# Kernel optimization log

Measured on AMD Instinct MI355X. Metric: run time of the kernel, lower is better.

Reference implementation:

```python
import jax, jax.numpy as jnp
import numpy as np

IN_FEATURES = 128
OUT_FEATURES = 64

def setup_inputs() -> dict:
    key = jax.random.key(0)
    k1, k2, k3 = jax.random.split(key, 3)
    x = jax.random.normal(k1, (8, 4096, IN_FEATURES), dtype=jnp.float32)
    # nn.Linear weights: W [out, in], a [1, 2*out]
    W = jax.random.normal(k2, (OUT_FEATURES, IN_FEATURES), dtype=jnp.float32) / np.sqrt(IN_FEATURES)
    a = jax.random.normal(k3, (1, 2 * OUT_FEATURES), dtype=jnp.float32) / np.sqrt(2 * OUT_FEATURES)
    return {"x": x, "W": W, "a": a}

def reference(x, W, a):
    # h = x @ W.T : [B, N, D]
    h = jnp.einsum('bnf,df->bnd', x, W)
    d = h.shape[-1]
    a1 = a[0, :d]  # [D]
    a2 = a[0, d:]  # [D]
    score1 = h @ a1  # [B, N]
    score2 = h @ a2  # [B, N]
    # outer-sum broadcast: e[b,i,j] = leakyrelu(score1[b,i] + score2[b,j])
    e = jax.nn.leaky_relu(score1[:, :, None] + score2[:, None, :], negative_slope=0.2)
    attention = jax.nn.softmax(e, axis=-1)  # [B, N, N]
    h_prime = jnp.einsum('bij,bjd->bid', attention, h)
    return jax.nn.elu(h_prime)
```

## Files before the change

### kernel.cpp

```cpp
#include <hip/hip_runtime.h>
#include <hip/hip_bf16.h>

#define BB 8
#define NN 4096
#define FF 128
#define DD 64
#define NB (BB*NN)
#define CHK 128
#define NCH (NN/CHK)
#define CSZ 16
#define NC16 (NN/CSZ)
#define CH 72

#define OFF_H     0
#define OFF_S1    (OFF_H    + (size_t)NB*DD*4)
#define OFF_S2    (OFF_S1   + (size_t)NB*4)
#define OFF_S2S   (OFF_S2   + (size_t)NB*4)
#define OFF_PERM  (OFF_S2S  + (size_t)NB*4)
#define OFF_WPOS  (OFF_PERM + (size_t)NB*4)
#define OFF_WNEG  (OFF_WPOS + (size_t)NB*4)
#define OFF_CT16  (OFF_WNEG + (size_t)NB*4)
#define OFF_CTS   (OFF_CT16 + (size_t)BB*NC16*2*CH*8)
#define OFF_PRANK (OFF_CTS  + (size_t)BB*(NC16+1)*2*CH*8)

__device__ __forceinline__ unsigned int fkey(float f) {
  unsigned int u = __float_as_uint(f);
  return (u & 0x80000000u) ? ~u : (u | 0x80000000u);
}

__global__ __launch_bounds__(256) void gat_kA(const float* __restrict__ x,
                                              const float* __restrict__ W,
                                              const float* __restrict__ a,
                                              float* __restrict__ h,
                                              float* __restrict__ s1,
                                              float* __restrict__ s2) {
  __shared__ float xs[64][FF];
  const int tid  = threadIdx.x;
  const int lane = tid & 63;
  const int wave = tid >> 6;
  const long long rowbase = (long long)blockIdx.x * 64;

  const float4* x4  = (const float4*)(x + rowbase * FF);
  float4*       xs4 = (float4*)&xs[0][0];
#pragma unroll
  for (int i = 0; i < 8; ++i) xs4[tid + i * 256] = x4[tid + i * 256];

  float4 wreg[32];
  const float4* W4 = (const float4*)(W + lane * FF);
#pragma unroll
  for (int j = 0; j < 32; ++j) wreg[j] = W4[j];
  const float a1d = a[lane];
  const float a2d = a[DD + lane];
  __syncthreads();

  for (int r = wave * 16; r < wave * 16 + 16; ++r) {
    const float4* xr = (const float4*)&xs[r][0];
    float4 acc = {0.f, 0.f, 0.f, 0.f};
#pragma unroll
    for (int j = 0; j < 32; ++j) {
      float4 xv = xr[j];
      acc.x += xv.x * wreg[j].x;
      acc.y += xv.y * wreg[j].y;
      acc.z += xv.z * wreg[j].z;
      acc.w += xv.w * wreg[j].w;
    }
    float hd = (acc.x + acc.y) + (acc.z + acc.w);
    const long long row = rowbase + r;
    h[row * DD + lane] = hd;

    float p1 = hd * a1d, p2 = hd * a2d;
#pragma unroll
    for (int o = 32; o; o >>= 1) { p1 += __shfl_xor(p1, o); p2 += __shfl_xor(p2, o); }
    if (lane == 0) { s1[row] = p1; s2[row] = p2; }
  }
}

__global__ __launch_bounds__(256) void gat_kB1(const float* __restrict__ s2,
                                               unsigned short* __restrict__ prank) {
  __shared__ unsigned long long ks[CHK];
  const int c = blockIdx.x, b = blockIdx.y, tid = threadIdx.x;
  const float* s2b = s2 + (size_t)b * NN;

  if (tid < CHK) {
    const int ig = c * CHK + tid;
    ks[tid] = ((unsigned long long)fkey(s2b[ig]) << 12) | (unsigned)ig;
  }

  unsigned long long kj[16];
  int rank[16];
#pragma unroll
  for (int t = 0; t < 16; ++t) {
    const int j = tid + 256 * t;
    kj[t] = ((unsigned long long)fkey(s2b[j]) << 12) | (unsigned)j;
    rank[t] = 0;
  }
  __syncthreads();

#pragma unroll 4
  for (int i = 0; i < CHK; ++i) {
    const unsigned long long ki = ks[i];
#pragma unroll
    for (int t = 0; t < 16; ++t) rank[t] += (ki < kj[t]) ? 1 : 0;
  }

  unsigned short* pr = prank + ((size_t)c * BB + b) * NN;
#pragma unroll
  for (int t = 0; t < 16; ++t) pr[tid + 256 * t] = (unsigned short)rank[t];
}

__global__ __launch_bounds__(256) void gat_kB2(const float* __restrict__ s2,
                                               const unsigned short* __restrict__ prank,
                                               float* __restrict__ s2s,
                                               int* __restrict__ perm,
                                               float* __restrict__ wpos,
                                               float* __restrict__ wneg) {
  __shared__ float red[4];
  const int b = blockIdx.y, tid = threadIdx.x;
  const int j = blockIdx.x * 256 + tid;
  const float* s2b = s2 + (size_t)b * NN;

  float mx = -3.4e38f;
  for (int i = tid; i < NN; i += 256) mx = fmaxf(mx, s2b[i]);
#pragma unroll
  for (int o = 32; o; o >>= 1) mx = fmaxf(mx, __shfl_xor(mx, o));
  if ((tid & 63) == 0) red[tid >> 6] = mx;
  __syncthreads();
  mx = fmaxf(fmaxf(red[0], red[1]), fmaxf(red[2], red[3]));

  int rank = 0;
#pragma unroll 8
  for (int c = 0; c < NCH; ++c) rank += prank[((size_t)c * BB + b) * NN + j];

  const float key = s2b[j];
  const size_t o = (size_t)b * NN + rank;
  s2s[o]  = key;
  perm[o] = j;
  wpos[o] = expf(key - mx);
  wneg[o] = expf(0.2f * (key - mx));
}

__global__ __launch_bounds__(64) void gat_kC(const float* __restrict__ h,
                                             const int* __restrict__ perm,
                                             const float* __restrict__ wpos,
                                             const float* __restrict__ wneg,
                                             double* __restrict__ CT16) {
  const int c = blockIdx.x, b = blockIdx.y, d = threadIdx.x;
  const int base = b * NN + c * CSZ;
  double ap = 0, an = 0, zp = 0, zn = 0;
#pragma unroll
  for (int s = 0; s < CSZ; ++s) {
    const int j  = base + s;
    const int pj = perm[j];
    const float hv = h[((size_t)b * NN + pj) * DD + d];
    const float wp = wpos[j], wn = wneg[j];
    ap += (double)wp * hv; an += (double)wn * hv;
    zp += wp;              zn += wn;
  }
  double* o = CT16 + ((size_t)(b * NC16 + c) * 2) * CH;
  o[0 * CH + d] = an;
  o[1 * CH + d] = ap;
  if (d == 0) { o[0 * CH + 64] = zn; o[1 * CH + 64] = zp; }
}

__global__ __launch_bounds__(256) void gat_kD(const double* __restrict__ CT16,
                                              double* __restrict__ CTS) {
  const int b = blockIdx.x, t = threadIdx.x;
  const int fam = t >> 7, ch = t & 127;
  if (ch > 64) return;
  double off = 0;
#pragma unroll 4
  for (int c = 0; c < NC16; ++c) {
    CTS[(((size_t)b * (NC16 + 1) + c) * 2 + fam) * CH + ch] = off;
    off += CT16[(((size_t)b * NC16 + c) * 2 + fam) * CH + ch];
  }
  CTS[(((size_t)b * (NC16 + 1) + NC16) * 2 + fam) * CH + ch] = off;
}

__global__ __launch_bounds__(256) void gat_kF(const float* __restrict__ s1,
                                              const float* __restrict__ s2s,
                                              const int* __restrict__ perm,
                                              const float* __restrict__ wpos,
                                              const float* __restrict__ wneg,
                                              const float* __restrict__ h,
                                              const double* __restrict__ CTS,
                                              float* __restrict__ out) {
  __shared__ float key[NN];
  __shared__ float seglast[64];
  const int b = blockIdx.y;
  const int tid = threadIdx.x, lane = tid & 63, wv = tid >> 6;

  const float4* src = (const float4*)(s2s + (size_t)b * NN);
  float4* dst = (float4*)key;
#pragma unroll
  for (int i = 0; i < 4; ++i) dst[tid + 256 * i] = src[tid + 256 * i];
  __syncthreads();
  if (tid < 64) seglast[tid] = key[tid * 64 + 63];
  __syncthreads();

  const float c1 = key[NN - 1];
  const double* base0 = CTS + ((size_t)b * (NC16 + 1)) * 2 * CH;
  const double* tt = base0 + (size_t)NC16 * 2 * CH + CH;
  const double tot = tt[lane];
  const double Zt  = tt[64];
  const int bNN = b * NN;
  const float segl = seglast[lane];

  for (int r = 0; r < 4; ++r) {
    const int rowl = blockIdx.x * 16 + wv * 4 + r;
    const long long row = (long long)bNN + rowl;
    const float s1i = s1[row];
    const float t = -s1i;

    unsigned long long m1 = __ballot(segl <= t);
    int seg = __popcll(m1); if (seg > 63) seg = 63;
    const float v2 = key[seg * 64 + lane];
    unsigned long long m2 = __ballot(v2 <= t);
    const int k = seg * 64 + __popcll(m2);
    const int c16 = k >> 4;

    const double* r0 = base0 + (size_t)c16 * 2 * CH;
    const double* r1 = r0 + CH;
    double pre  = r0[lane];
    double p1v  = r1[lane];
    double Zpre = r0[64];
    double Z1   = r1[64];

    for (int j = (c16 << 4); j < k; ++j) {
      const int pj = perm[bNN + j];
      const float hv = h[((size_t)(bNN + pj)) * DD + lane];
      const float wp = wpos[bNN + j], wn = wneg[bNN + j];
      pre += (double)wn * hv; p1v += (double)wp * hv;
      Zpre += wn;             Z1 += wp;
    }

    const float suf_d = (float)(tot - p1v);
    const float Zsuf  = (float)(Zt - Z1);
    const float z = s1i + c1;
    const float m = z >= 0.f ? z : 0.2f * z;
    const float A  = expf(z - m);
    const float Bn = expf(0.2f * z - m);
    const float num = A * suf_d + Bn * (float)pre;
    const float Z   = A * Zsuf  + Bn * (float)Zpre;
    const float hp  = num / Z;
    out[row * DD + lane] = hp > 0.f ? hp : expm1f(hp);
  }
}

extern "C" void kernel_launch(void* const* d_in, const int* in_sizes, int n_in,
                              void* d_out, int out_size, void* d_ws, size_t ws_size,
                              hipStream_t stream) {
  const float* x = (const float*)d_in[0];
  const float* W = (const float*)d_in[1];
  const float* a = (const float*)d_in[2];
  float* out = (float*)d_out;

  char* ws = (char*)d_ws;
  float*  h    = (float*)(ws + OFF_H);
  float*  s1   = (float*)(ws + OFF_S1);
  float*  s2   = (float*)(ws + OFF_S2);
  float*  s2s  = (float*)(ws + OFF_S2S);
  int*    perm = (int*)  (ws + OFF_PERM);
  float*  wpos = (float*)(ws + OFF_WPOS);
  float*  wneg = (float*)(ws + OFF_WNEG);
  double* CT16 = (double*)(ws + OFF_CT16);
  double* CTS  = (double*)(ws + OFF_CTS);
  unsigned short* prank = (unsigned short*)(ws + OFF_PRANK);

  gat_kA<<<NB / 64, 256, 0, stream>>>(x, W, a, h, s1, s2);
  gat_kB1<<<dim3(NCH, BB), 256, 0, stream>>>(s2, prank);
  gat_kB2<<<dim3(NN / 256, BB), 256, 0, stream>>>(s2, prank, s2s, perm, wpos, wneg);
  gat_kC<<<dim3(NC16, BB), 64, 0, stream>>>(h, perm, wpos, wneg, CT16);
  gat_kD<<<BB, 256, 0, stream>>>(CT16, CTS);
  gat_kF<<<dim3(NN / 16, BB), 256, 0, stream>>>(s1, s2s, perm, wpos, wneg, h, CTS, out);
}
```

Before: 101.8 us.

## Pack perm and weight into int2, derive wpos from wneg, unroll tail loop

```diff
diff --git a/kernel.cpp b/kernel.cpp
--- a/kernel.cpp
+++ b/kernel.cpp
@@ -16,10 +16,8 @@
 #define OFF_S1    (OFF_H    + (size_t)NB*DD*4)
 #define OFF_S2    (OFF_S1   + (size_t)NB*4)
 #define OFF_S2S   (OFF_S2   + (size_t)NB*4)
-#define OFF_PERM  (OFF_S2S  + (size_t)NB*4)
-#define OFF_WPOS  (OFF_PERM + (size_t)NB*4)
-#define OFF_WNEG  (OFF_WPOS + (size_t)NB*4)
-#define OFF_CT16  (OFF_WNEG + (size_t)NB*4)
+#define OFF_PK    (OFF_S2S  + (size_t)NB*4)
+#define OFF_CT16  (OFF_PK   + (size_t)NB*8)
 #define OFF_CTS   (OFF_CT16 + (size_t)BB*NC16*2*CH*8)
 #define OFF_PRANK (OFF_CTS  + (size_t)BB*(NC16+1)*2*CH*8)
 
@@ -111,9 +109,7 @@
 __global__ __launch_bounds__(256) void gat_kB2(const float* __restrict__ s2,
                                                const unsigned short* __restrict__ prank,
                                                float* __restrict__ s2s,
-                                               int* __restrict__ perm,
-                                               float* __restrict__ wpos,
-                                               float* __restrict__ wneg) {
+                                               int2* __restrict__ pk) {
   __shared__ float red[4];
   const int b = blockIdx.y, tid = threadIdx.x;
   const int j = blockIdx.x * 256 + tid;
@@ -132,29 +128,27 @@
   for (int c = 0; c < NCH; ++c) rank += prank[((size_t)c * BB + b) * NN + j];
 
   const float key = s2b[j];
+  const float wn = expf(0.2f * (key - mx));
   const size_t o = (size_t)b * NN + rank;
-  s2s[o]  = key;
-  perm[o] = j;
-  wpos[o] = expf(key - mx);
-  wneg[o] = expf(0.2f * (key - mx));
+  s2s[o] = key;
+  pk[o]  = make_int2(j, __float_as_int(wn));
 }
 
 __global__ __launch_bounds__(64) void gat_kC(const float* __restrict__ h,
-                                             const int* __restrict__ perm,
-                                             const float* __restrict__ wpos,
-                                             const float* __restrict__ wneg,
+                                             const int2* __restrict__ pk,
                                              double* __restrict__ CT16) {
   const int c = blockIdx.x, b = blockIdx.y, d = threadIdx.x;
   const int base = b * NN + c * CSZ;
   double ap = 0, an = 0, zp = 0, zn = 0;
 #pragma unroll
   for (int s = 0; s < CSZ; ++s) {
-    const int j  = base + s;
-    const int pj = perm[j];
-    const float hv = h[((size_t)b * NN + pj) * DD + d];
-    const float wp = wpos[j], wn = wneg[j];
-    ap += (double)wp * hv; an += (double)wn * hv;
-    zp += wp;              zn += wn;
+    const int2 p = pk[base + s];
+    const float hv = h[((size_t)(b * NN + p.x)) * DD + d];
+    const float wn = __int_as_float(p.y);
+    const float w2 = wn * wn;
+    const float wp = w2 * w2 * wn;
+    an += (double)wn * hv; ap += (double)wp * hv;
+    zn += wn;              zp += wp;
   }
   double* o = CT16 + ((size_t)(b * NC16 + c) * 2) * CH;
   o[0 * CH + d] = an;
@@ -162,13 +156,12 @@
   if (d == 0) { o[0 * CH + 64] = zn; o[1 * CH + 64] = zp; }
 }
 
-__global__ __launch_bounds__(256) void gat_kD(const double* __restrict__ CT16,
+__global__ __launch_bounds__(128) void gat_kD(const double* __restrict__ CT16,
                                               double* __restrict__ CTS) {
-  const int b = blockIdx.x, t = threadIdx.x;
-  const int fam = t >> 7, ch = t & 127;
+  const int b = blockIdx.x, fam = blockIdx.y, ch = threadIdx.x;
   if (ch > 64) return;
   double off = 0;
-#pragma unroll 4
+#pragma unroll 16
   for (int c = 0; c < NC16; ++c) {
     CTS[(((size_t)b * (NC16 + 1) + c) * 2 + fam) * CH + ch] = off;
     off += CT16[(((size_t)b * NC16 + c) * 2 + fam) * CH + ch];
@@ -178,9 +171,7 @@
 
 __global__ __launch_bounds__(256) void gat_kF(const float* __restrict__ s1,
                                               const float* __restrict__ s2s,
-                                              const int* __restrict__ perm,
-                                              const float* __restrict__ wpos,
-                                              const float* __restrict__ wneg,
+                                              const int2* __restrict__ pk,
                                               const float* __restrict__ h,
                                               const double* __restrict__ CTS,
                                               float* __restrict__ out) {
@@ -197,26 +188,29 @@
   if (tid < 64) seglast[tid] = key[tid * 64 + 63];
   __syncthreads();
 
+  const int bNN = b * NN;
   const float c1 = key[NN - 1];
   const double* base0 = CTS + ((size_t)b * (NC16 + 1)) * 2 * CH;
   const double* tt = base0 + (size_t)NC16 * 2 * CH + CH;
   const double tot = tt[lane];
   const double Zt  = tt[64];
-  const int bNN = b * NN;
   const float segl = seglast[lane];
 
+  float s1v[4];
+#pragma unroll
+  for (int r = 0; r < 4; ++r) s1v[r] = s1[bNN + blockIdx.x * 16 + wv * 4 + r];
+
+#pragma unroll
   for (int r = 0; r < 4; ++r) {
     const int rowl = blockIdx.x * 16 + wv * 4 + r;
-    const long long row = (long long)bNN + rowl;
-    const float s1i = s1[row];
+    const float s1i = s1v[r];
     const float t = -s1i;
 
     unsigned long long m1 = __ballot(segl <= t);
     int seg = __popcll(m1); if (seg > 63) seg = 63;
     const float v2 = key[seg * 64 + lane];
-    unsigned long long m2 = __ballot(v2 <= t);
-    const int k = seg * 64 + __popcll(m2);
-    const int c16 = k >> 4;
+    const int k = seg * 64 + __popcll(__ballot(v2 <= t));
+    const int c16 = k >> 4, cnt = k & 15;
 
     const double* r0 = base0 + (size_t)c16 * 2 * CH;
     const double* r1 = r0 + CH;
@@ -225,12 +219,18 @@
     double Zpre = r0[64];
     double Z1   = r1[64];
 
-    for (int j = (c16 << 4); j < k; ++j) {
-      const int pj = perm[bNN + j];
-      const float hv = h[((size_t)(bNN + pj)) * DD + lane];
-      const float wp = wpos[bNN + j], wn = wneg[bNN + j];
+    const int j0 = c16 << 4;
+#pragma unroll
+    for (int jj = 0; jj < 15; ++jj) {
+      int jn = j0 + jj; jn = jn < NN ? jn : NN - 1;
+      const int2 p = pk[bNN + jn];
+      const float hv = h[((size_t)(bNN + p.x)) * DD + lane];
+      const float msk = (jj < cnt) ? 1.0f : 0.0f;
+      const float wn = __int_as_float(p.y) * msk;
+      const float w2 = wn * wn;
+      const float wp = w2 * w2 * wn * msk;
       pre += (double)wn * hv; p1v += (double)wp * hv;
-      Zpre += wn;             Z1 += wp;
+      Zpre += wn;             Z1  += wp;
     }
 
     const float suf_d = (float)(tot - p1v);
@@ -242,7 +242,7 @@
     const float num = A * suf_d + Bn * (float)pre;
     const float Z   = A * Zsuf  + Bn * (float)Zpre;
     const float hp  = num / Z;
-    out[row * DD + lane] = hp > 0.f ? hp : expm1f(hp);
+    out[((size_t)(bNN + rowl)) * DD + lane] = hp > 0.f ? hp : expm1f(hp);
   }
 }
 
@@ -259,17 +259,15 @@
   float*  s1   = (float*)(ws + OFF_S1);
   float*  s2   = (float*)(ws + OFF_S2);
   float*  s2s  = (float*)(ws + OFF_S2S);
-  int*    perm = (int*)  (ws + OFF_PERM);
-  float*  wpos = (float*)(ws + OFF_WPOS);
-  float*  wneg = (float*)(ws + OFF_WNEG);
+  int2*   pk   = (int2*) (ws + OFF_PK);
   double* CT16 = (double*)(ws + OFF_CT16);
   double* CTS  = (double*)(ws + OFF_CTS);
   unsigned short* prank = (unsigned short*)(ws + OFF_PRANK);
 
   gat_kA<<<NB / 64, 256, 0, stream>>>(x, W, a, h, s1, s2);
   gat_kB1<<<dim3(NCH, BB), 256, 0, stream>>>(s2, prank);
-  gat_kB2<<<dim3(NN / 256, BB), 256, 0, stream>>>(s2, prank, s2s, perm, wpos, wneg);
-  gat_kC<<<dim3(NC16, BB), 64, 0, stream>>>(h, perm, wpos, wneg, CT16);
-  gat_kD<<<BB, 256, 0, stream>>>(CT16, CTS);
-  gat_kF<<<dim3(NN / 16, BB), 256, 0, stream>>>(s1, s2s, perm, wpos, wneg, h, CTS, out);
-}
+  gat_kB2<<<dim3(NN / 256, BB), 256, 0, stream>>>(s2, prank, s2s, pk);
+  gat_kC<<<dim3(NC16, BB), 64, 0, stream>>>(h, pk, CT16);
+  gat_kD<<<dim3(BB, 2), 128, 0, stream>>>(CT16, CTS);
+  gat_kF<<<dim3(NN / 16, BB), 256, 0, stream>>>(s1, s2s, pk, h, CTS, out);
+}
```

After: 85.78 us. 1.19x faster.
